# Kernel optimization log

Hardware: AMD Instinct MI355X
Metric: run time of the kernel (lower is better)

## Reference

```python
import jax, jax.numpy as jnp
import numpy as np

QLEN, MLEN, BSZ = 1024, 1024, 4
D, H, DH, DFF, L, V = 512, 8, 64, 2048, 3, 32000


def layer_norm(x, g, b, eps=1e-5):
    mu = jnp.mean(x, axis=-1, keepdims=True)
    var = jnp.var(x, axis=-1, keepdims=True)
    return (x - mu) * jax.lax.rsqrt(var + eps) * g + b


def setup_inputs() -> dict:
    key = jax.random.key(0)
    ks = jax.random.split(key, 16)
    s = 0.02
    return {
        "inp": jax.random.randint(ks[0], (QLEN, BSZ), 0, V, dtype=jnp.int32),
        "emb": jax.random.normal(ks[1], (V, D), jnp.float32) * s,
        "mems": jax.random.normal(ks[2], (L, MLEN, BSZ, D), jnp.float32) * s,
        "Wq": jax.random.normal(ks[3], (L, D, H * DH), jnp.float32) * s,
        "Wkv": jax.random.normal(ks[4], (L, D, 2 * H * DH), jnp.float32) * s,
        "Wo": jax.random.normal(ks[5], (L, H * DH, D), jnp.float32) * s,
        "ln1_g": jnp.ones((L, D), jnp.float32),
        "ln1_b": jnp.zeros((L, D), jnp.float32),
        "W1": jax.random.normal(ks[6], (L, D, DFF), jnp.float32) * s,
        "b1": jnp.zeros((L, DFF), jnp.float32),
        "W2": jax.random.normal(ks[7], (L, DFF, D), jnp.float32) * s,
        "b2": jnp.zeros((L, D), jnp.float32),
        "ln2_g": jnp.ones((L, D), jnp.float32),
        "ln2_b": jnp.zeros((L, D), jnp.float32),
    }


def reference(inp, emb, mems, Wq, Wkv, Wo, ln1_g, ln1_b, W1, b1, W2, b2, ln2_g, ln2_b):
    qlen, bsz = inp.shape
    mlen = mems.shape[1]
    klen = mlen + qlen
    scale = 1.0 / np.sqrt(DH).astype(np.float32)

    # adaptive embedding (div_val=1, d_proj==d_embed): lookup * sqrt(d_proj)
    h = emb[inp] * np.sqrt(D).astype(np.float32)  # [qlen, bsz, D]

    # absolute sinusoidal positional embedding over klen, last qlen positions added
    inv_freq = 1.0 / (10000.0 ** (jnp.arange(0, D, 2, dtype=jnp.float32) / D))
    pos_seq = jnp.arange(klen - 1, -1, -1, dtype=jnp.float32)
    sinusoid = pos_seq[:, None] * inv_freq[None, :]  # [klen, D/2]
    pos_emb = jnp.concatenate([jnp.sin(sinusoid), jnp.cos(sinusoid)], axis=-1)
    h = h + pos_emb[-qlen:, None, :]

    # causal mask with memory: query i attends keys j <= i + mlen
    mask = jnp.arange(klen)[None, :] > (jnp.arange(qlen)[:, None] + mlen)  # [qlen, klen]

    for l in range(L):
        c = jnp.concatenate([mems[l], h], axis=0)  # [klen, bsz, D]
        q = (h @ Wq[l]).reshape(qlen, bsz, H, DH)
        kv = c @ Wkv[l]
        k, v = jnp.split(kv, 2, axis=-1)
        k = k.reshape(klen, bsz, H, DH)
        v = v.reshape(klen, bsz, H, DH)
        score = jnp.einsum('ibnd,jbnd->ijbn', q, k) * scale
        score = jnp.where(mask[:, :, None, None], -jnp.inf, score)
        prob = jax.nn.softmax(score, axis=1)
        vec = jnp.einsum('ijbn,jbnd->ibnd', prob, v).reshape(qlen, bsz, H * DH)
        h = layer_norm(h + vec @ Wo[l], ln1_g[l], ln1_b[l])
        ff = jax.nn.relu(h @ W1[l] + b1[l]) @ W2[l] + b2[l]
        h = layer_norm(h + ff, ln2_g[l], ln2_b[l])
    return h
```

## Files before the change

### kernel.cpp

```cpp
#include <hip/hip_runtime.h>
#include <hip/hip_bf16.h>

#define QLEN_ 1024
#define MLEN_ 1024
#define BSZ_ 4
#define DM_ 512
#define NH_ 8
#define DFF_ 2048
#define NLAYER_ 3

typedef __bf16 bf16x8_t __attribute__((ext_vector_type(8)));
typedef float f32x4_t __attribute__((ext_vector_type(4)));
typedef unsigned short u16x4 __attribute__((ext_vector_type(4)));
typedef unsigned short u16x8 __attribute__((ext_vector_type(8)));

__device__ __forceinline__ unsigned short f2bf(float x) {
  __hip_bfloat16 h = __float2bfloat16(x);
  return __builtin_bit_cast(unsigned short, h);
}
__device__ __forceinline__ float bf2f(unsigned short u) {
  return __uint_as_float(((unsigned)u) << 16);
}
__device__ __forceinline__ void gll16(const void* g, void* l) {
  __builtin_amdgcn_global_load_lds(
      (const __attribute__((address_space(1))) void*)g,
      (__attribute__((address_space(3))) void*)l, 16, 0, 0);
}

__global__ __launch_bounds__(256) void transpose_cvt(
    const float* __restrict__ src, unsigned short* __restrict__ dst,
    int K, int N, int sstride, int dstride)
{
  __shared__ float t[32][33];
  src += (size_t)sstride * blockIdx.z;
  dst += (size_t)dstride * blockIdx.z;
  const int n0 = blockIdx.x * 32, k0 = blockIdx.y * 32;
  const int tx = threadIdx.x, ty = threadIdx.y;
#pragma unroll
  for (int i = ty; i < 32; i += 8)
    t[i][tx] = src[(size_t)(k0 + i) * N + n0 + tx];
  __syncthreads();
#pragma unroll
  for (int i = ty; i < 32; i += 8)
    dst[(size_t)(n0 + i) * K + k0 + tx] = f2bf(t[tx][i]);
}

__global__ __launch_bounds__(256) void cvt_mems(
    const float* __restrict__ mems, unsigned short* __restrict__ cb)
{
  const int l = blockIdx.z;
  const int e = (blockIdx.x * 256 + threadIdx.x) * 4;
  const float4 v = *(const float4*)(mems + (size_t)l * 2097152 + e);
  u16x4 o = { f2bf(v.x), f2bf(v.y), f2bf(v.z), f2bf(v.w) };
  *(u16x4*)(cb + (size_t)l * 4194304 + e) = o;
}

__global__ __launch_bounds__(256) void embed_kernel(
    const int* __restrict__ inp, const float* __restrict__ emb,
    float* __restrict__ h, unsigned short* __restrict__ hb)
{
  const int row = blockIdx.x;
  const int i = row >> 2;
  const int tok = inp[row];
  const float pv = (float)(QLEN_ - 1 - i);
  for (int d = threadIdx.x; d < DM_; d += 256) {
    const int j = (d < 256) ? d : d - 256;
    const float invf = __expf(-((2.0f * j) / 512.0f) * 9.210340371976184f);
    const float ang = pv * invf;
    const float pos = (d < 256) ? sinf(ang) : cosf(ang);
    const float v = emb[(size_t)tok * DM_ + d] * 22.627416997969522f + pos;
    h[(size_t)row * DM_ + d] = v;
    hb[(size_t)row * DM_ + d] = f2bf(v);
  }
}

template<int BM, int OUT_BF16, int HAS_BIAS, int DO_RELU>
__global__ __launch_bounds__(256) void gemm_bt(
    const unsigned short* __restrict__ A, const unsigned short* __restrict__ BT,
    void* __restrict__ Cv, const float* __restrict__ bias, int M, int N, int K)
{
  constexpr int MFR = BM / 32;
  __shared__ unsigned short As[BM * 64];
  __shared__ unsigned short Bs[128 * 64];
  const int tid = threadIdx.x;
  const int lane = tid & 63;
  const int w = tid >> 6;
  const int wm = w >> 1, wn = w & 1;
  const int tm = blockIdx.x, tn = blockIdx.y;

  f32x4_t zero = {0.f, 0.f, 0.f, 0.f};
  f32x4_t acc[MFR][4];
#pragma unroll
  for (int i = 0; i < MFR; i++)
#pragma unroll
    for (int j = 0; j < 4; j++) acc[i][j] = zero;

  const int srow = tid >> 3;
  const int schunk = (tid & 7) ^ (srow & 7);
  const unsigned short* ap = A + (size_t)(tm * BM + srow) * K + schunk * 8;
  const unsigned short* bp = BT + (size_t)(tn * 128 + srow) * K + schunk * 8;
  unsigned short* lA = As + tid * 8;
  unsigned short* lB = Bs + tid * 8;
  const size_t k32 = (size_t)32 * K;

  for (int k0 = 0; k0 < K; k0 += 64) {
#pragma unroll
    for (int ii = 0; ii < BM / 32; ii++) gll16(ap + ii * k32, lA + ii * 2048);
#pragma unroll
    for (int ii = 0; ii < 4; ii++) gll16(bp + ii * k32, lB + ii * 2048);
    ap += 64; bp += 64;
    __syncthreads();
    const int fr = lane & 15;
    const int lg = lane >> 4;
    bf16x8_t af[MFR][2], bg[4][2];
#pragma unroll
    for (int i = 0; i < MFR; i++) {
      const int r = wm * (BM / 2) + i * 16 + fr;
#pragma unroll
      for (int ks = 0; ks < 2; ks++)
        af[i][ks] = *(const bf16x8_t*)(As + r * 64 + (((ks << 2) + lg) ^ (r & 7)) * 8);
    }
#pragma unroll
    for (int j = 0; j < 4; j++) {
      const int r = wn * 64 + j * 16 + fr;
#pragma unroll
      for (int ks = 0; ks < 2; ks++)
        bg[j][ks] = *(const bf16x8_t*)(Bs + r * 64 + (((ks << 2) + lg) ^ (r & 7)) * 8);
    }
#pragma unroll
    for (int ks = 0; ks < 2; ks++)
#pragma unroll
      for (int i = 0; i < MFR; i++)
#pragma unroll
        for (int j = 0; j < 4; j++)
          acc[i][j] = __builtin_amdgcn_mfma_f32_16x16x32_bf16(af[i][ks], bg[j][ks], acc[i][j], 0, 0, 0);
    __syncthreads();
  }

  const int row0 = tm * BM + wm * (BM / 2) + ((lane >> 4) << 2);
  const int col0 = tn * 128 + wn * 64 + (lane & 15);
#pragma unroll
  for (int i = 0; i < MFR; i++) {
#pragma unroll
    for (int j = 0; j < 4; j++) {
      const int c = col0 + j * 16;
      const float bv = HAS_BIAS ? bias[c] : 0.0f;
#pragma unroll
      for (int r = 0; r < 4; r++) {
        float v = acc[i][j][r] + bv;
        if (DO_RELU) v = fmaxf(v, 0.0f);
        const size_t off = (size_t)(row0 + i * 16 + r) * N + c;
        if (OUT_BF16) ((unsigned short*)Cv)[off] = f2bf(v);
        else          ((float*)Cv)[off] = v;
      }
    }
  }
}

__global__ __launch_bounds__(256) void attn_mfma(
    const unsigned short* __restrict__ qkv, unsigned short* __restrict__ vec)
{
  __shared__ unsigned short Klds[2][64 * 64];
  __shared__ unsigned short Vt[2][64 * 64];
  __shared__ unsigned short Plds[4][16 * 64];

  const int tid = threadIdx.x;
  const int lane = tid & 63;
  const int w = tid >> 6;
  const int b = blockIdx.y >> 3;
  const int hh = blockIdx.y & 7;
  const int i0 = blockIdx.x * 64;
  const int lg = lane >> 4;
  const int lr = lane & 15;

  bf16x8_t qf[2];
  {
    const unsigned short* qp = qkv + (size_t)(4096 + (i0 + w * 16 + lr) * 4 + b) * 1536 + hh * 64 + lg * 8;
    qf[0] = *(const bf16x8_t*)qp;
    qf[1] = *(const bf16x8_t*)(qp + 32);
  }

  const f32x4_t zero4 = {0.f, 0.f, 0.f, 0.f};
  f32x4_t oacc[4];
#pragma unroll
  for (int j = 0; j < 4; j++) oacc[j] = zero4;
  float lrow[4] = {0.f, 0.f, 0.f, 0.f};

  const int ntiles = 17 + blockIdx.x;

  const int kc0 = tid, kc1 = tid + 256;
  const int krow0 = kc0 >> 3, kcc0 = (kc0 & 7) ^ (krow0 & 7);
  const int krow1 = kc1 >> 3, kcc1 = (kc1 & 7) ^ (krow1 & 7);
  const int vkey = lane;
  const int vdc0 = w, vdc1 = w + 4;

  const unsigned short* kbase = qkv + (size_t)b * 1536 + 512 + hh * 64;
  const unsigned short* vbase = qkv + (size_t)b * 1536 + 1024 + hh * 64;

  u16x8 va0 = *(const u16x8*)(vbase + (size_t)vkey * 6144 + vdc0 * 8);
  u16x8 va1 = *(const u16x8*)(vbase + (size_t)vkey * 6144 + vdc1 * 8);
  gll16(kbase + (size_t)krow0 * 6144 + kcc0 * 8, (char*)Klds[0] + kc0 * 16);
  gll16(kbase + (size_t)krow1 * 6144 + kcc1 * 8, (char*)Klds[0] + kc1 * 16);

  int cur = 0;
  for (int t = 0; t < ntiles; t++) {
    unsigned short* vtc = Vt[cur];
#pragma unroll
    for (int u = 0; u < 8; u++) {
      const int d0 = vdc0 * 8 + u;
      vtc[d0 * 64 + ((((vkey >> 3) ^ (d0 & 7)) << 3) | (vkey & 7))] = (unsigned short)va0[u];
    }
#pragma unroll
    for (int u = 0; u < 8; u++) {
      const int d1 = vdc1 * 8 + u;
      vtc[d1 * 64 + ((((vkey >> 3) ^ (d1 & 7)) << 3) | (vkey & 7))] = (unsigned short)va1[u];
    }
    __syncthreads();

    if (t + 1 < ntiles) {
      const unsigned short* kt = kbase + (size_t)(t + 1) * 64 * 6144;
      const unsigned short* vt = vbase + (size_t)((t + 1) * 64 + vkey) * 6144;
      va0 = *(const u16x8*)(vt + vdc0 * 8);
      va1 = *(const u16x8*)(vt + vdc1 * 8);
      gll16(kt + (size_t)krow0 * 6144 + kcc0 * 8, (char*)Klds[cur ^ 1] + kc0 * 16);
      gll16(kt + (size_t)krow1 * 6144 + kcc1 * 8, (char*)Klds[cur ^ 1] + kc1 * 16);
    }

    f32x4_t s[4];
#pragma unroll
    for (int n = 0; n < 4; n++) s[n] = zero4;
    __builtin_amdgcn_s_setprio(1);
#pragma unroll
    for (int ks = 0; ks < 2; ks++) {
#pragma unroll
      for (int n = 0; n < 4; n++) {
        const int kr = 16 * n + lr;
        const bf16x8_t kg = *(const bf16x8_t*)((const char*)Klds[cur] + kr * 128 +
                                               ((((ks << 2) + lg) ^ (kr & 7)) << 4));
        s[n] = __builtin_amdgcn_mfma_f32_16x16x32_bf16(qf[ks], kg, s[n], 0, 0, 0);
      }
    }
    __builtin_amdgcn_s_setprio(0);

#pragma unroll
    for (int r = 0; r < 4; r++) {
      const int prow = lg * 4 + r;
      const int jlim = i0 + w * 16 + prow + MLEN_ - t * 64;
      unsigned short* pw = Plds[w] + prow * 64;
      float ls = 0.f;
#pragma unroll
      for (int n = 0; n < 4; n++) {
        const int key = lr + 16 * n;
        float pv = __expf(s[n][r] * 0.125f);
        pv = (key <= jlim) ? pv : 0.f;
        ls += pv;
        pw[(((key >> 3) ^ (prow & 7)) << 3) | (key & 7)] = f2bf(pv);
      }
      lrow[r] += ls;
    }

    __builtin_amdgcn_s_setprio(1);
#pragma unroll
    for (int ks = 0; ks < 2; ks++) {
      const bf16x8_t pf = *(const bf16x8_t*)((const char*)Plds[w] + lr * 128 +
                                             ((((ks << 2) + lg) ^ (lr & 7)) << 4));
#pragma unroll
      for (int jj = 0; jj < 4; jj++) {
        const int vr = 16 * jj + lr;
        const bf16x8_t vg = *(const bf16x8_t*)((const char*)Vt[cur] + vr * 128 +
                                               ((((ks << 2) + lg) ^ (vr & 7)) << 4));
        oacc[jj] = __builtin_amdgcn_mfma_f32_16x16x32_bf16(pf, vg, oacc[jj], 0, 0, 0);
      }
    }
    __builtin_amdgcn_s_setprio(0);
    cur ^= 1;
  }

#pragma unroll
  for (int r = 0; r < 4; r++) {
    float ls = lrow[r];
    ls += __shfl_xor(ls, 1); ls += __shfl_xor(ls, 2);
    ls += __shfl_xor(ls, 4); ls += __shfl_xor(ls, 8);
    const float inv = 1.0f / ls;
    const int row = i0 + w * 16 + lg * 4 + r;
    unsigned short* op = vec + ((size_t)row * BSZ_ + b) * 512 + hh * 64 + lr;
#pragma unroll
    for (int jj = 0; jj < 4; jj++) op[16 * jj] = f2bf(oacc[jj][r] * inv);
  }
}

__global__ __launch_bounds__(256) void add_ln(
    const float* __restrict__ x1, const float* __restrict__ x2,
    const float* __restrict__ g, const float* __restrict__ bb,
    float* __restrict__ outf, unsigned short* __restrict__ outb)
{
  const int row = blockIdx.x;
  const int tid = threadIdx.x;
  const size_t base = (size_t)row * DM_;
  const float v0 = x1[base + tid] + x2[base + tid];
  const float v1 = x1[base + tid + 256] + x2[base + tid + 256];
  float s = v0 + v1;
  float ss = v0 * v0 + v1 * v1;
#pragma unroll
  for (int o = 32; o; o >>= 1) { s += __shfl_xor(s, o); ss += __shfl_xor(ss, o); }
  __shared__ float rs[4], rss[4];
  if ((tid & 63) == 0) { rs[tid >> 6] = s; rss[tid >> 6] = ss; }
  __syncthreads();
  s = rs[0] + rs[1] + rs[2] + rs[3];
  ss = rss[0] + rss[1] + rss[2] + rss[3];
  const float mu = s * (1.0f / 512.0f);
  const float var = ss * (1.0f / 512.0f) - mu * mu;
  const float rstd = rsqrtf(var + 1e-5f);
  const float o0 = (v0 - mu) * rstd * g[tid] + bb[tid];
  const float o1 = (v1 - mu) * rstd * g[tid + 256] + bb[tid + 256];
  outf[base + tid] = o0;
  outf[base + tid + 256] = o1;
  outb[base + tid] = f2bf(o0);
  outb[base + tid + 256] = f2bf(o1);
}

extern "C" void kernel_launch(void* const* d_in, const int* in_sizes, int n_in,
                              void* d_out, int out_size, void* d_ws, size_t ws_size,
                              hipStream_t stream) {
  (void)in_sizes; (void)n_in; (void)out_size; (void)ws_size;
  const int*   inp   = (const int*)d_in[0];
  const float* emb   = (const float*)d_in[1];
  const float* mems  = (const float*)d_in[2];
  const float* Wq    = (const float*)d_in[3];
  const float* Wkv   = (const float*)d_in[4];
  const float* Wo    = (const float*)d_in[5];
  const float* ln1g  = (const float*)d_in[6];
  const float* ln1b  = (const float*)d_in[7];
  const float* W1    = (const float*)d_in[8];
  const float* b1    = (const float*)d_in[9];
  const float* W2    = (const float*)d_in[10];
  const float* b2    = (const float*)d_in[11];
  const float* ln2g  = (const float*)d_in[12];
  const float* ln2b  = (const float*)d_in[13];

  char* p = (char*)d_ws;
  float*          h     = (float*)p;          p += (size_t)8 << 20;
  float*          h2    = (float*)p;          p += (size_t)8 << 20;
  unsigned short* cb    = (unsigned short*)p; p += (size_t)24 << 20;
  unsigned short* qkvb  = (unsigned short*)p; p += (size_t)24 << 20;
  unsigned short* vecb  = (unsigned short*)p; p += (size_t)4 << 20;
  unsigned short* WqkvT = (unsigned short*)p; p += (size_t)3 * 1536 * 512 * 2;
  unsigned short* WoT   = (unsigned short*)p; p += (size_t)3 * 512 * 512 * 2;
  unsigned short* W1T   = (unsigned short*)p; p += (size_t)3 * 2048 * 512 * 2;
  unsigned short* W2T   = (unsigned short*)p; p += (size_t)3 * 512 * 2048 * 2;
  float*          s2  = (float*)qkvb;
  unsigned short* s1  = qkvb + (size_t)4 * 1024 * 1024;
  unsigned short* h2b = vecb;

  transpose_cvt<<<dim3(16, 16, 3), dim3(32, 8), 0, stream>>>(Wq,  WqkvT,             512, 512,  512 * 512,  1536 * 512);
  transpose_cvt<<<dim3(32, 16, 3), dim3(32, 8), 0, stream>>>(Wkv, WqkvT + 512 * 512, 512, 1024, 512 * 1024, 1536 * 512);
  transpose_cvt<<<dim3(16, 16, 3), dim3(32, 8), 0, stream>>>(Wo,  WoT,  512, 512,  512 * 512,  512 * 512);
  transpose_cvt<<<dim3(64, 16, 3), dim3(32, 8), 0, stream>>>(W1,  W1T,  512, 2048, 512 * 2048, 2048 * 512);
  transpose_cvt<<<dim3(16, 64, 3), dim3(32, 8), 0, stream>>>(W2,  W2T,  2048, 512, 2048 * 512, 512 * 2048);
  cvt_mems<<<dim3(2048, 1, 3), 256, 0, stream>>>(mems, cb);
  embed_kernel<<<QLEN_ * BSZ_, 256, 0, stream>>>(inp, emb, h, cb + 2097152);

  for (int l = 0; l < NLAYER_; l++) {
    gemm_bt<128, 1, 0, 0><<<dim3(64, 12), 256, 0, stream>>>(
        cb + (size_t)l * 4194304, WqkvT + (size_t)l * 786432, qkvb, nullptr, 8192, 1536, 512);
    attn_mfma<<<dim3(16, 32), 256, 0, stream>>>(qkvb, vecb);
    gemm_bt<64, 0, 0, 0><<<dim3(64, 4), 256, 0, stream>>>(
        vecb, WoT + (size_t)l * 262144, s2, nullptr, 4096, 512, 512);
    add_ln<<<4096, 256, 0, stream>>>(h, s2, ln1g + l * 512, ln1b + l * 512, h2, h2b);
    gemm_bt<128, 1, 1, 1><<<dim3(32, 16), 256, 0, stream>>>(
        h2b, W1T + (size_t)l * 1048576, s1, b1 + l * 2048, 4096, 2048, 512);
    gemm_bt<64, 0, 1, 0><<<dim3(64, 4), 256, 0, stream>>>(
        s1, W2T + (size_t)l * 1048576, s2, b2 + l * 512, 4096, 512, 2048);
    float* outp = (l == NLAYER_ - 1) ? (float*)d_out : h;
    unsigned short* outb = (l < NLAYER_ - 1) ? (cb + (size_t)(l + 1) * 4194304 + 2097152)
                                             : (cb + 2097152);
    add_ln<<<4096, 256, 0, stream>>>(h2, s2, ln2g + l * 512, ln2b + l * 512, outp, outb);
  }
}
```

Before: 630.1 us.

## Process 128 query rows per attention block to reuse K/V tiles across two row blocks

```diff
diff --git a/kernel.cpp b/kernel.cpp
--- a/kernel.cpp
+++ b/kernel.cpp
@@ -162,31 +162,34 @@
 {
   __shared__ unsigned short Klds[2][64 * 64];
   __shared__ unsigned short Vt[2][64 * 64];
-  __shared__ unsigned short Plds[4][16 * 64];
+  __shared__ unsigned short Plds[4][32 * 64];
 
   const int tid = threadIdx.x;
   const int lane = tid & 63;
   const int w = tid >> 6;
-  const int b = blockIdx.y >> 3;
-  const int hh = blockIdx.y & 7;
-  const int i0 = blockIdx.x * 64;
+  const int b = blockIdx.x >> 3;
+  const int hh = blockIdx.x & 7;
+  const int i0 = blockIdx.y * 128;
   const int lg = lane >> 4;
   const int lr = lane & 15;
 
-  bf16x8_t qf[2];
-  {
-    const unsigned short* qp = qkv + (size_t)(4096 + (i0 + w * 16 + lr) * 4 + b) * 1536 + hh * 64 + lg * 8;
-    qf[0] = *(const bf16x8_t*)qp;
-    qf[1] = *(const bf16x8_t*)(qp + 32);
+  bf16x8_t qf[2][2];
+#pragma unroll
+  for (int rb = 0; rb < 2; rb++) {
+    const unsigned short* qp = qkv + (size_t)(4096 + (i0 + w * 32 + rb * 16 + lr) * 4 + b) * 1536 + hh * 64 + lg * 8;
+    qf[rb][0] = *(const bf16x8_t*)qp;
+    qf[rb][1] = *(const bf16x8_t*)(qp + 32);
   }
 
   const f32x4_t zero4 = {0.f, 0.f, 0.f, 0.f};
-  f32x4_t oacc[4];
-#pragma unroll
-  for (int j = 0; j < 4; j++) oacc[j] = zero4;
-  float lrow[4] = {0.f, 0.f, 0.f, 0.f};
-
-  const int ntiles = 17 + blockIdx.x;
+  f32x4_t oacc[2][4];
+#pragma unroll
+  for (int rb = 0; rb < 2; rb++)
+#pragma unroll
+    for (int j = 0; j < 4; j++) oacc[rb][j] = zero4;
+  float lrow[2][4] = {{0.f, 0.f, 0.f, 0.f}, {0.f, 0.f, 0.f, 0.f}};
+
+  const int ntiles = 18 + 2 * blockIdx.y;
 
   const int kc0 = tid, kc1 = tid + 256;
   const int krow0 = kc0 >> 3, kcc0 = (kc0 & 7) ^ (krow0 & 7);
@@ -226,9 +229,11 @@
       gll16(kt + (size_t)krow1 * 6144 + kcc1 * 8, (char*)Klds[cur ^ 1] + kc1 * 16);
     }
 
-    f32x4_t s[4];
-#pragma unroll
-    for (int n = 0; n < 4; n++) s[n] = zero4;
+    f32x4_t s[2][4];
+#pragma unroll
+    for (int rb = 0; rb < 2; rb++)
+#pragma unroll
+      for (int n = 0; n < 4; n++) s[rb][n] = zero4;
     __builtin_amdgcn_s_setprio(1);
 #pragma unroll
     for (int ks = 0; ks < 2; ks++) {
@@ -237,39 +242,51 @@
         const int kr = 16 * n + lr;
         const bf16x8_t kg = *(const bf16x8_t*)((const char*)Klds[cur] + kr * 128 +
                                                ((((ks << 2) + lg) ^ (kr & 7)) << 4));
-        s[n] = __builtin_amdgcn_mfma_f32_16x16x32_bf16(qf[ks], kg, s[n], 0, 0, 0);
+#pragma unroll
+        for (int rb = 0; rb < 2; rb++)
+          s[rb][n] = __builtin_amdgcn_mfma_f32_16x16x32_bf16(qf[rb][ks], kg, s[rb][n], 0, 0, 0);
       }
     }
     __builtin_amdgcn_s_setprio(0);
 
 #pragma unroll
-    for (int r = 0; r < 4; r++) {
-      const int prow = lg * 4 + r;
-      const int jlim = i0 + w * 16 + prow + MLEN_ - t * 64;
-      unsigned short* pw = Plds[w] + prow * 64;
-      float ls = 0.f;
-#pragma unroll
-      for (int n = 0; n < 4; n++) {
-        const int key = lr + 16 * n;
-        float pv = __expf(s[n][r] * 0.125f);
-        pv = (key <= jlim) ? pv : 0.f;
-        ls += pv;
-        pw[(((key >> 3) ^ (prow & 7)) << 3) | (key & 7)] = f2bf(pv);
-      }
-      lrow[r] += ls;
+    for (int rb = 0; rb < 2; rb++) {
+#pragma unroll
+      for (int r = 0; r < 4; r++) {
+        const int prow = rb * 16 + lg * 4 + r;
+        const int jlim = i0 + w * 32 + prow + MLEN_ - t * 64;
+        unsigned short* pw = Plds[w] + prow * 64;
+        float ls = 0.f;
+#pragma unroll
+        for (int n = 0; n < 4; n++) {
+          const int key = lr + 16 * n;
+          float pv = __expf(s[rb][n][r] * 0.125f);
+          pv = (key <= jlim) ? pv : 0.f;
+          ls += pv;
+          pw[(((key >> 3) ^ (prow & 7)) << 3) | (key & 7)] = f2bf(pv);
+        }
+        lrow[rb][r] += ls;
+      }
     }
 
     __builtin_amdgcn_s_setprio(1);
 #pragma unroll
     for (int ks = 0; ks < 2; ks++) {
-      const bf16x8_t pf = *(const bf16x8_t*)((const char*)Plds[w] + lr * 128 +
-                                             ((((ks << 2) + lg) ^ (lr & 7)) << 4));
+      bf16x8_t pf[2];
+#pragma unroll
+      for (int rb = 0; rb < 2; rb++) {
+        const int pr = rb * 16 + lr;
+        pf[rb] = *(const bf16x8_t*)((const char*)Plds[w] + pr * 128 +
+                                    ((((ks << 2) + lg) ^ (pr & 7)) << 4));
+      }
 #pragma unroll
       for (int jj = 0; jj < 4; jj++) {
         const int vr = 16 * jj + lr;
         const bf16x8_t vg = *(const bf16x8_t*)((const char*)Vt[cur] + vr * 128 +
                                                ((((ks << 2) + lg) ^ (vr & 7)) << 4));
-        oacc[jj] = __builtin_amdgcn_mfma_f32_16x16x32_bf16(pf, vg, oacc[jj], 0, 0, 0);
+#pragma unroll
+        for (int rb = 0; rb < 2; rb++)
+          oacc[rb][jj] = __builtin_amdgcn_mfma_f32_16x16x32_bf16(pf[rb], vg, oacc[rb][jj], 0, 0, 0);
       }
     }
     __builtin_amdgcn_s_setprio(0);
@@ -277,15 +294,18 @@
   }
 
 #pragma unroll
-  for (int r = 0; r < 4; r++) {
-    float ls = lrow[r];
-    ls += __shfl_xor(ls, 1); ls += __shfl_xor(ls, 2);
-    ls += __shfl_xor(ls, 4); ls += __shfl_xor(ls, 8);
-    const float inv = 1.0f / ls;
-    const int row = i0 + w * 16 + lg * 4 + r;
-    unsigned short* op = vec + ((size_t)row * BSZ_ + b) * 512 + hh * 64 + lr;
-#pragma unroll
-    for (int jj = 0; jj < 4; jj++) op[16 * jj] = f2bf(oacc[jj][r] * inv);
+  for (int rb = 0; rb < 2; rb++) {
+#pragma unroll
+    for (int r = 0; r < 4; r++) {
+      float ls = lrow[rb][r];
+      ls += __shfl_xor(ls, 1); ls += __shfl_xor(ls, 2);
+      ls += __shfl_xor(ls, 4); ls += __shfl_xor(ls, 8);
+      const float inv = 1.0f / ls;
+      const int row = i0 + w * 32 + rb * 16 + lg * 4 + r;
+      unsigned short* op = vec + ((size_t)row * BSZ_ + b) * 512 + hh * 64 + lr;
+#pragma unroll
+      for (int jj = 0; jj < 4; jj++) op[16 * jj] = f2bf(oacc[rb][jj][r] * inv);
+    }
   }
 }
 
@@ -363,7 +383,7 @@
   for (int l = 0; l < NLAYER_; l++) {
     gemm_bt<128, 1, 0, 0><<<dim3(64, 12), 256, 0, stream>>>(
         cb + (size_t)l * 4194304, WqkvT + (size_t)l * 786432, qkvb, nullptr, 8192, 1536, 512);
-    attn_mfma<<<dim3(16, 32), 256, 0, stream>>>(qkvb, vecb);
+    attn_mfma<<<dim3(32, 8), 256, 0, stream>>>(qkvb, vecb);
     gemm_bt<64, 0, 0, 0><<<dim3(64, 4), 256, 0, stream>>>(
         vecb, WoT + (size_t)l * 262144, s2, nullptr, 4096, 512, 512);
     add_ln<<<4096, 256, 0, stream>>>(h, s2, ln1g + l * 512, ln1b + l * 512, h2, h2b);
```

New measurement: 664.1 us. +5.4%, slower.

## Fold softmax scale into Q projection and transpose score MFMA in attention

Applied to the files above, without the earlier changes.

```diff
diff --git a/kernel.cpp b/kernel.cpp
--- a/kernel.cpp
+++ b/kernel.cpp
@@ -20,6 +20,11 @@
 }
 __device__ __forceinline__ float bf2f(unsigned short u) {
   return __uint_as_float(((unsigned)u) << 16);
+}
+__device__ __forceinline__ unsigned cvtpk(float lo, float hi) {
+  unsigned r;
+  asm("v_cvt_pk_bf16_f32 %0, %1, %2" : "=v"(r) : "v"(lo), "v"(hi));
+  return r;
 }
 __device__ __forceinline__ void gll16(const void* g, void* l) {
   __builtin_amdgcn_global_load_lds(
@@ -74,7 +79,7 @@
   }
 }
 
-template<int BM, int OUT_BF16, int HAS_BIAS, int DO_RELU>
+template<int BM, int OUT_BF16, int HAS_BIAS, int DO_RELU, int QSCALE>
 __global__ __launch_bounds__(256) void gemm_bt(
     const unsigned short* __restrict__ A, const unsigned short* __restrict__ BT,
     void* __restrict__ Cv, const float* __restrict__ bias, int M, int N, int K)
@@ -148,6 +153,7 @@
 #pragma unroll
       for (int r = 0; r < 4; r++) {
         float v = acc[i][j][r] + bv;
+        if (QSCALE && c < 512) v *= 0.18033688011112042f;
         if (DO_RELU) v = fmaxf(v, 0.0f);
         const size_t off = (size_t)(row0 + i * 16 + r) * N + c;
         if (OUT_BF16) ((unsigned short*)Cv)[off] = f2bf(v);
@@ -167,9 +173,9 @@
   const int tid = threadIdx.x;
   const int lane = tid & 63;
   const int w = tid >> 6;
-  const int b = blockIdx.y >> 3;
-  const int hh = blockIdx.y & 7;
-  const int i0 = blockIdx.x * 64;
+  const int b = blockIdx.x >> 3;
+  const int hh = blockIdx.x & 7;
+  const int i0 = blockIdx.y * 64;
   const int lg = lane >> 4;
   const int lr = lane & 15;
 
@@ -184,9 +190,9 @@
   f32x4_t oacc[4];
 #pragma unroll
   for (int j = 0; j < 4; j++) oacc[j] = zero4;
-  float lrow[4] = {0.f, 0.f, 0.f, 0.f};
-
-  const int ntiles = 17 + blockIdx.x;
+  float lrow = 0.f;
+
+  const int ntiles = 17 + blockIdx.y;
 
   const int kc0 = tid, kc1 = tid + 256;
   const int krow0 = kc0 >> 3, kcc0 = (kc0 & 7) ^ (krow0 & 7);
@@ -237,26 +243,38 @@
         const int kr = 16 * n + lr;
         const bf16x8_t kg = *(const bf16x8_t*)((const char*)Klds[cur] + kr * 128 +
                                                ((((ks << 2) + lg) ^ (kr & 7)) << 4));
-        s[n] = __builtin_amdgcn_mfma_f32_16x16x32_bf16(qf[ks], kg, s[n], 0, 0, 0);
+        s[n] = __builtin_amdgcn_mfma_f32_16x16x32_bf16(kg, qf[ks], s[n], 0, 0, 0);
       }
     }
     __builtin_amdgcn_s_setprio(0);
 
-#pragma unroll
-    for (int r = 0; r < 4; r++) {
-      const int prow = lg * 4 + r;
-      const int jlim = i0 + w * 16 + prow + MLEN_ - t * 64;
-      unsigned short* pw = Plds[w] + prow * 64;
-      float ls = 0.f;
-#pragma unroll
-      for (int n = 0; n < 4; n++) {
-        const int key = lr + 16 * n;
-        float pv = __expf(s[n][r] * 0.125f);
-        pv = (key <= jlim) ? pv : 0.f;
-        ls += pv;
-        pw[(((key >> 3) ^ (prow & 7)) << 3) | (key & 7)] = f2bf(pv);
-      }
-      lrow[r] += ls;
+    float pe[4][4];
+    const bool nomask = (t * 64 + 63 <= i0 + w * 16 + MLEN_);
+    if (nomask) {
+#pragma unroll
+      for (int n = 0; n < 4; n++)
+#pragma unroll
+        for (int r = 0; r < 4; r++) pe[n][r] = __builtin_exp2f(s[n][r]);
+    } else {
+      const int jlim = i0 + w * 16 + lr + MLEN_ - t * 64;
+#pragma unroll
+      for (int n = 0; n < 4; n++)
+#pragma unroll
+        for (int r = 0; r < 4; r++) {
+          const float e = __builtin_exp2f(s[n][r]);
+          pe[n][r] = (16 * n + 4 * lg + r <= jlim) ? e : 0.f;
+        }
+    }
+    lrow += ((pe[0][0] + pe[0][1]) + (pe[0][2] + pe[0][3]))
+          + ((pe[1][0] + pe[1][1]) + (pe[1][2] + pe[1][3]))
+          + ((pe[2][0] + pe[2][1]) + (pe[2][2] + pe[2][3]))
+          + ((pe[3][0] + pe[3][1]) + (pe[3][2] + pe[3][3]));
+    char* pwb = (char*)Plds[w] + lr * 128 + (lg & 1) * 8;
+#pragma unroll
+    for (int n = 0; n < 4; n++) {
+      const int cp = (2 * n + (lg >> 1)) ^ (lr & 7);
+      *(unsigned*)(pwb + cp * 16 + 0) = cvtpk(pe[n][0], pe[n][1]);
+      *(unsigned*)(pwb + cp * 16 + 4) = cvtpk(pe[n][2], pe[n][3]);
     }
 
     __builtin_amdgcn_s_setprio(1);
@@ -276,16 +294,16 @@
     cur ^= 1;
   }
 
+  lrow += __shfl_xor(lrow, 16);
+  lrow += __shfl_xor(lrow, 32);
+  const float inv = 1.0f / lrow;
 #pragma unroll
   for (int r = 0; r < 4; r++) {
-    float ls = lrow[r];
-    ls += __shfl_xor(ls, 1); ls += __shfl_xor(ls, 2);
-    ls += __shfl_xor(ls, 4); ls += __shfl_xor(ls, 8);
-    const float inv = 1.0f / ls;
+    const float invr = __shfl(inv, lg * 4 + r);
     const int row = i0 + w * 16 + lg * 4 + r;
     unsigned short* op = vec + ((size_t)row * BSZ_ + b) * 512 + hh * 64 + lr;
 #pragma unroll
-    for (int jj = 0; jj < 4; jj++) op[16 * jj] = f2bf(oacc[jj][r] * inv);
+    for (int jj = 0; jj < 4; jj++) op[16 * jj] = f2bf(oacc[jj][r] * invr);
   }
 }
 
@@ -361,15 +379,15 @@
   embed_kernel<<<QLEN_ * BSZ_, 256, 0, stream>>>(inp, emb, h, cb + 2097152);
 
   for (int l = 0; l < NLAYER_; l++) {
-    gemm_bt<128, 1, 0, 0><<<dim3(64, 12), 256, 0, stream>>>(
+    gemm_bt<128, 1, 0, 0, 1><<<dim3(64, 12), 256, 0, stream>>>(
         cb + (size_t)l * 4194304, WqkvT + (size_t)l * 786432, qkvb, nullptr, 8192, 1536, 512);
-    attn_mfma<<<dim3(16, 32), 256, 0, stream>>>(qkvb, vecb);
-    gemm_bt<64, 0, 0, 0><<<dim3(64, 4), 256, 0, stream>>>(
+    attn_mfma<<<dim3(32, 16), 256, 0, stream>>>(qkvb, vecb);
+    gemm_bt<64, 0, 0, 0, 0><<<dim3(64, 4), 256, 0, stream>>>(
         vecb, WoT + (size_t)l * 262144, s2, nullptr, 4096, 512, 512);
     add_ln<<<4096, 256, 0, stream>>>(h, s2, ln1g + l * 512, ln1b + l * 512, h2, h2b);
-    gemm_bt<128, 1, 1, 1><<<dim3(32, 16), 256, 0, stream>>>(
+    gemm_bt<128, 1, 1, 1, 0><<<dim3(32, 16), 256, 0, stream>>>(
         h2b, W1T + (size_t)l * 1048576, s1, b1 + l * 2048, 4096, 2048, 512);
-    gemm_bt<64, 0, 1, 0><<<dim3(64, 4), 256, 0, stream>>>(
+    gemm_bt<64, 0, 1, 0, 0><<<dim3(64, 4), 256, 0, stream>>>(
         s1, W2T + (size_t)l * 1048576, s2, b2 + l * 512, 4096, 512, 2048);
     float* outp = (l == NLAYER_ - 1) ? (float*)d_out : h;
     unsigned short* outb = (l < NLAYER_ - 1) ? (cb + (size_t)(l + 1) * 4194304 + 2097152)
```

Measured after the change: 607.6 us. 3.6% less time.
